# Optimization experiments

Measured on AMD Instinct MI355X. Metric: run time of the kernel, lower is better.

Reference implementation:

```python
import jax, jax.numpy as jnp
import numpy as np

B, D, E, K = 8192, 1024, 8, 5  # batch, in_dim, num_size_classes, num_depth_classes
H = max(64, D)                 # hidden = max(64, in_dim)
EPS = 1e-8


def ordinal_logits_to_probs(logits, num_classes):
    # logits: [B, K-1] cumulative ordinal logits -> [B, K] class probs
    q = jax.nn.sigmoid(logits)
    probs = jnp.concatenate(
        [1.0 - q[:, :1], q[:, :-1] - q[:, 1:], q[:, -1:]], axis=1
    )  # [B, K]
    probs = jnp.clip(probs, EPS)
    return probs / jnp.clip(probs.sum(axis=1, keepdims=True), EPS)


def setup_inputs() -> dict:
    key = jax.random.key(0)
    kx, ks, k1, k2 = jax.random.split(key, 4)
    x = jax.random.normal(kx, (B, D), dtype=jnp.float32)
    size_idx = jax.random.randint(ks, (B,), 0, E, dtype=jnp.int64)
    # per-expert 2-layer MLP params: Linear(D,H) -> ReLU -> Linear(H,K-1)
    W1 = jax.random.normal(k1, (E, D, H), dtype=jnp.float32) / np.sqrt(D)
    b1 = jnp.zeros((E, H), dtype=jnp.float32)
    W2 = jax.random.normal(k2, (E, H, K - 1), dtype=jnp.float32) / np.sqrt(H)
    b2 = jnp.zeros((E, K - 1), dtype=jnp.float32)
    return {"x": x, "size_idx": size_idx, "W1": W1, "b1": b1, "W2": W2, "b2": b2}


def reference(x, size_idx, W1, b1, W2, b2):
    # Hard routing: each token gets the output of expert size_idx[b].
    # Dense all-expert compute + per-token select (same math as mask/gather/scatter,
    # dropout is inference-mode identity).
    h = jax.nn.relu(jnp.einsum('bd,edh->beh', x, W1) + b1)      # [B, E, H]
    all_logits = jnp.einsum('beh,ehk->bek', h, W2) + b2          # [B, E, K-1]
    idx = size_idx.astype(jnp.int32)[:, None, None]              # [B, 1, 1]
    logits = jnp.take_along_axis(all_logits, idx, axis=1)[:, 0]  # [B, K-1]
    probs = ordinal_logits_to_probs(logits, K)                   # [B, K]
    return logits, probs
```

## Files before the change

kernel.cpp:

```cpp
#include <hip/hip_runtime.h>
#include <cstdint>
#include <cstddef>

#define Bn 8192
#define Dn 1024
#define Hn 1024
#define En 8
#define MT 128
#define NB 16
#define MTILES (Bn / MT + En)
#define PERM_N (Bn + En * MT)

typedef unsigned short u16;
typedef __bf16 bf16x8 __attribute__((ext_vector_type(8)));
typedef float f32x4 __attribute__((ext_vector_type(4)));
typedef unsigned short ushort8 __attribute__((ext_vector_type(8)));

__device__ __forceinline__ u16 f2bf(float f) {
  unsigned int u = __float_as_uint(f);
  unsigned int r = u + 0x7fffu + ((u >> 16) & 1u);
  return (u16)(r >> 16);
}

__device__ __forceinline__ void gld16(const void* g, void* l) {
  __builtin_amdgcn_global_load_lds(
      (const __attribute__((address_space(1))) void*)g,
      (__attribute__((address_space(3))) void*)l, 16, 0, 0);
}

#define PIPE_BARRIER_VM4() do {                    \
    asm volatile("" ::: "memory");                 \
    __builtin_amdgcn_s_waitcnt(0x0F74);            \
    __builtin_amdgcn_s_barrier();                  \
    asm volatile("" ::: "memory");                 \
  } while (0)
#define PIPE_BARRIER_VM0() do {                    \
    asm volatile("" ::: "memory");                 \
    __builtin_amdgcn_s_waitcnt(0x0F70);            \
    __builtin_amdgcn_s_barrier();                  \
    asm volatile("" ::: "memory");                 \
  } while (0)

__global__ __launch_bounds__(1024) void route_k(const int* __restrict__ sidx,
                                                int* __restrict__ off,
                                                int* __restrict__ perm) {
  __shared__ int hist[16][En];
  __shared__ int base[16][En];
  __shared__ int eoff[En + 1];
  int t = threadIdx.x;
  int wv = t >> 6;
  if (t < 16 * En) ((int*)hist)[t] = 0;
#pragma unroll
  for (int i = 0; i < PERM_N / 1024; i++) perm[t + i * 1024] = -1;
  __syncthreads();
  int e8[8], r8[8];
#pragma unroll
  for (int i = 0; i < 8; i++) {
    int e = sidx[t + i * 1024];
    e8[i] = e;
    r8[i] = atomicAdd(&hist[wv][e], 1);
  }
  __syncthreads();
  if (t < En) {
    int s = 0;
    for (int w = 0; w < 16; w++) { base[w][t] = s; s += hist[w][t]; }
    hist[0][t] = s;
  }
  __syncthreads();
  if (t == 0) {
    int o = 0;
    for (int e = 0; e < En; e++) {
      eoff[e] = o; off[e] = o;
      o += (hist[0][e] + MT - 1) & ~(MT - 1);
    }
    eoff[En] = o; off[En] = o;
  }
  __syncthreads();
#pragma unroll
  for (int i = 0; i < 8; i++) {
    int e = e8[i];
    perm[eoff[e] + base[wv][e] + r8[i]] = t + i * 1024;
  }
}

__global__ __launch_bounds__(256) void cvt_xp_k(const float* __restrict__ x,
                                                const int* __restrict__ perm,
                                                u16* __restrict__ xbp) {
  size_t idx = ((size_t)blockIdx.x * 256 + threadIdx.x) * 8;
  int p = (int)(idx >> 10);
  int col = (int)(idx & 1023);
  int tok = perm[p];
  ushort8 o;
  if (tok < 0) {
    o = (ushort8){0, 0, 0, 0, 0, 0, 0, 0};
  } else {
    const float* src = x + ((size_t)tok << 10) + col;
    float4 a = *(const float4*)src;
    float4 b = *(const float4*)(src + 4);
    o[0] = f2bf(a.x); o[1] = f2bf(a.y); o[2] = f2bf(a.z); o[3] = f2bf(a.w);
    o[4] = f2bf(b.x); o[5] = f2bf(b.y); o[6] = f2bf(b.z); o[7] = f2bf(b.w);
  }
  *(ushort8*)(xbp + idx) = o;
}

__global__ __launch_bounds__(256) void cvt_w1_k(const float* __restrict__ W1,
                                                u16* __restrict__ W1t) {
  __shared__ float tile[64][65];
  int e = blockIdx.z;
  int k0 = blockIdx.y * 64;
  int n0 = blockIdx.x * 64;
  int c4 = (threadIdx.x & 15) * 4;
  int r0 = threadIdx.x >> 4;
  const float* src = W1 + ((size_t)e << 20) + (size_t)k0 * Hn + n0;
#pragma unroll
  for (int i = 0; i < 4; i++) {
    int r = r0 + i * 16;
    float4 v = *(const float4*)(src + (size_t)r * Hn + c4);
    tile[r][c4 + 0] = v.x; tile[r][c4 + 1] = v.y;
    tile[r][c4 + 2] = v.z; tile[r][c4 + 3] = v.w;
  }
  __syncthreads();
  u16* dst = W1t + ((size_t)e << 20) + (size_t)n0 * Dn + k0;
#pragma unroll
  for (int i = 0; i < 4; i++) {
    int h = r0 + i * 16;
    ushort4 o;
    o.x = f2bf(tile[c4 + 0][h]);
    o.y = f2bf(tile[c4 + 1][h]);
    o.z = f2bf(tile[c4 + 2][h]);
    o.w = f2bf(tile[c4 + 3][h]);
    *(ushort4*)(dst + (size_t)h * Dn + c4) = o;
  }
}

__global__ __launch_bounds__(256) void gemm_k(
    const u16* __restrict__ xbp, const u16* __restrict__ w1t,
    const float* __restrict__ b1, const float* __restrict__ w2,
    const int* __restrict__ off, float* __restrict__ partials) {
  __shared__ u16 As[3][4096];
  __shared__ u16 Bs[3][4096];

  int n0 = blockIdx.x * 128;
  int row0 = blockIdx.y * MT;
  if (row0 >= off[En]) return;
  int e = 0;
  while (row0 >= off[e + 1]) e++;

  int tid = threadIdx.x;
  int lane = tid & 63, w = tid >> 6;
  int wm = w >> 1, wn = w & 1;

  int srow = lane >> 2;
  int slot = lane & 3;
  int scol = (slot ^ ((srow >> 1) & 3)) * 8;
  const u16* aG[2]; const u16* bG[2];
  int lOff[2];
#pragma unroll
  for (int j = 0; j < 2; j++) {
    int rl = 32 * w + 16 * j + srow;
    aG[j] = xbp + (size_t)(row0 + rl) * Dn + scol;
    bG[j] = w1t + ((size_t)e << 20) + (size_t)(n0 + rl) * Dn + scol;
    lOff[j] = (32 * w + 16 * j) * 32;
  }

  f32x4 acc[4][4];
#pragma unroll
  for (int i = 0; i < 4; i++)
#pragma unroll
    for (int j = 0; j < 4; j++)
      acc[i][j] = (f32x4){0.f, 0.f, 0.f, 0.f};

  int fr = lane & 15;
  int qf = lane >> 4;
  int qs = (qf ^ ((fr >> 1) & 3)) * 8;
  int offA[4], offB[4];
#pragma unroll
  for (int i = 0; i < 4; i++)
    offA[i] = (wm * 64 + i * 16 + fr) * 32 + qs;
#pragma unroll
  for (int j = 0; j < 4; j++)
    offB[j] = (wn * 64 + j * 16 + fr) * 32 + qs;

#pragma unroll
  for (int it = 0; it < 2; it++) {
    int ko = it * 32;
    gld16(aG[0] + ko, (u16*)As[it] + lOff[0]);
    gld16(aG[1] + ko, (u16*)As[it] + lOff[1]);
    gld16(bG[0] + ko, (u16*)Bs[it] + lOff[0]);
    gld16(bG[1] + ko, (u16*)Bs[it] + lOff[1]);
  }

#pragma unroll
  for (int i = 0; i < 31; i++) {
    PIPE_BARRIER_VM4();
    if (i + 2 < 32) {
      int s = (i + 2) % 3;
      int ko = (i + 2) * 32;
      gld16(aG[0] + ko, (u16*)As[s] + lOff[0]);
      gld16(aG[1] + ko, (u16*)As[s] + lOff[1]);
      gld16(bG[0] + ko, (u16*)Bs[s] + lOff[0]);
      gld16(bG[1] + ko, (u16*)Bs[s] + lOff[1]);
    }
    const u16* Ab = (const u16*)As[i % 3];
    const u16* Bb = (const u16*)Bs[i % 3];
    bf16x8 af[4], bfr[4];
#pragma unroll
    for (int ii = 0; ii < 4; ii++) af[ii] = *(const bf16x8*)(Ab + offA[ii]);
#pragma unroll
    for (int jj = 0; jj < 4; jj++) bfr[jj] = *(const bf16x8*)(Bb + offB[jj]);
#pragma unroll
    for (int ii = 0; ii < 4; ii++)
#pragma unroll
      for (int jj = 0; jj < 4; jj++)
        acc[ii][jj] = __builtin_amdgcn_mfma_f32_16x16x32_bf16(af[ii], bfr[jj], acc[ii][jj], 0, 0, 0);
  }
  {
    PIPE_BARRIER_VM0();
    const u16* Ab = (const u16*)As[31 % 3];
    const u16* Bb = (const u16*)Bs[31 % 3];
    bf16x8 af[4], bfr[4];
#pragma unroll
    for (int ii = 0; ii < 4; ii++) af[ii] = *(const bf16x8*)(Ab + offA[ii]);
#pragma unroll
    for (int jj = 0; jj < 4; jj++) bfr[jj] = *(const bf16x8*)(Bb + offB[jj]);
#pragma unroll
    for (int ii = 0; ii < 4; ii++)
#pragma unroll
      for (int jj = 0; jj < 4; jj++)
        acc[ii][jj] = __builtin_amdgcn_mfma_f32_16x16x32_bf16(af[ii], bfr[jj], acc[ii][jj], 0, 0, 0);
  }

  int fq = lane >> 4;
  float4 w2v[4]; float b1v[4];
#pragma unroll
  for (int j = 0; j < 4; j++) {
    int col = n0 + wn * 64 + j * 16 + fr;
    w2v[j] = *(const float4*)(w2 + ((size_t)e * Hn + col) * 4);
    b1v[j] = b1[(size_t)e * Hn + col];
  }
  int chunk = blockIdx.x * 2 + wn;
#pragma unroll
  for (int i = 0; i < 4; i++) {
    int rbase = wm * 64 + i * 16 + fq * 4;
#pragma unroll
    for (int r = 0; r < 4; r++) {
      float s0 = 0.f, s1 = 0.f, s2 = 0.f, s3 = 0.f;
#pragma unroll
      for (int j = 0; j < 4; j++) {
        float h = acc[i][j][r] + b1v[j];
        h = fmaxf(h, 0.f);
        s0 = fmaf(h, w2v[j].x, s0);
        s1 = fmaf(h, w2v[j].y, s1);
        s2 = fmaf(h, w2v[j].z, s2);
        s3 = fmaf(h, w2v[j].w, s3);
      }
#pragma unroll
      for (int m = 1; m < 16; m <<= 1) {
        s0 += __shfl_xor(s0, m);
        s1 += __shfl_xor(s1, m);
        s2 += __shfl_xor(s2, m);
        s3 += __shfl_xor(s3, m);
      }
      if (fr == 0) {
        int row = row0 + rbase + r;
        *(float4*)(partials + ((size_t)row * NB + chunk) * 4) =
            make_float4(s0, s1, s2, s3);
      }
    }
  }
}

__global__ void probs_k(const float* __restrict__ partials,
                        const int* __restrict__ perm, const int* __restrict__ off,
                        const int* __restrict__ sidx, const float* __restrict__ b2,
                        float* __restrict__ out) {
  int p = blockIdx.x * blockDim.x + threadIdx.x;
  if (p >= off[En]) return;
  int tok = perm[p];
  if (tok < 0) return;
  int e = sidx[tok];
  float s0 = 0.f, s1 = 0.f, s2 = 0.f, s3 = 0.f;
#pragma unroll
  for (int nb = 0; nb < NB; nb++) {
    float4 v = *(const float4*)(partials + ((size_t)p * NB + nb) * 4);
    s0 += v.x; s1 += v.y; s2 += v.z; s3 += v.w;
  }
  float l0 = s0 + b2[e * 4 + 0];
  float l1 = s1 + b2[e * 4 + 1];
  float l2 = s2 + b2[e * 4 + 2];
  float l3 = s3 + b2[e * 4 + 3];
  out[tok * 4 + 0] = l0; out[tok * 4 + 1] = l1;
  out[tok * 4 + 2] = l2; out[tok * 4 + 3] = l3;
  float q0 = 1.f / (1.f + expf(-l0));
  float q1 = 1.f / (1.f + expf(-l1));
  float q2 = 1.f / (1.f + expf(-l2));
  float q3 = 1.f / (1.f + expf(-l3));
  const float eps = 1e-8f;
  float p0 = fmaxf(1.f - q0, eps);
  float p1 = fmaxf(q0 - q1, eps);
  float p2 = fmaxf(q1 - q2, eps);
  float p3 = fmaxf(q2 - q3, eps);
  float p4 = fmaxf(q3, eps);
  float s = p0 + p1 + p2 + p3 + p4;
  float inv = 1.f / fmaxf(s, eps);
  float* pr = out + (size_t)Bn * 4 + (size_t)tok * 5;
  pr[0] = p0 * inv; pr[1] = p1 * inv; pr[2] = p2 * inv;
  pr[3] = p3 * inv; pr[4] = p4 * inv;
}

extern "C" void kernel_launch(void* const* d_in, const int* in_sizes, int n_in,
                              void* d_out, int out_size, void* d_ws, size_t ws_size,
                              hipStream_t stream) {
  const float* x  = (const float*)d_in[0];
  const int* sidx = (const int*)d_in[1];
  const float* W1 = (const float*)d_in[2];
  const float* b1 = (const float*)d_in[3];
  const float* W2 = (const float*)d_in[4];
  const float* b2 = (const float*)d_in[5];
  float* out = (float*)d_out;

  uint8_t* w = (uint8_t*)d_ws;
  int* off  = (int*)(w + 64);
  int* perm = (int*)(w + 512);
  u16* xbp      = (u16*)(w + 40960);
  u16* w1t      = (u16*)(w + 18919424);
  float* parts  = (float*)(w + 35700736);

  route_k<<<1, 1024, 0, stream>>>(sidx, off, perm);
  cvt_xp_k<<<(PERM_N * Dn) / (256 * 8), 256, 0, stream>>>(x, perm, xbp);
  cvt_w1_k<<<dim3(Hn / 64, Dn / 64, En), 256, 0, stream>>>(W1, w1t);
  gemm_k<<<dim3(Hn / 128, MTILES), 256, 0, stream>>>(xbp, w1t, b1, W2, off, parts);
  probs_k<<<(PERM_N + 255) / 256, 256, 0, stream>>>(parts, perm, off, sidx, b2, out);
}
```

Before: 160.6 us.

## Fuse prep kernels, gather tokens in GEMM, finalize probs via last-block atomics

```diff
diff --git a/kernel.cpp b/kernel.cpp
--- a/kernel.cpp
+++ b/kernel.cpp
@@ -7,9 +7,16 @@
 #define Hn 1024
 #define En 8
 #define MT 128
-#define NB 16
-#define MTILES (Bn / MT + En)
+#define MTILES (PERM_N / MT)
 #define PERM_N (Bn + En * MT)
+
+#define NXB 4096
+#define NWB 2048
+#define NZB 32
+#define XB0 1
+#define WB0 (XB0 + NXB)
+#define ZB0 (WB0 + NWB)
+#define TOTB (ZB0 + NZB)
 
 typedef unsigned short u16;
 typedef __bf16 bf16x8 __attribute__((ext_vector_type(8)));
@@ -41,107 +48,109 @@
     asm volatile("" ::: "memory");                 \
   } while (0)
 
-__global__ __launch_bounds__(1024) void route_k(const int* __restrict__ sidx,
-                                                int* __restrict__ off,
-                                                int* __restrict__ perm) {
-  __shared__ int hist[16][En];
-  __shared__ int base[16][En];
-  __shared__ int eoff[En + 1];
+__global__ __launch_bounds__(256) void prep_k(
+    const float* __restrict__ x, const int* __restrict__ sidx,
+    const float* __restrict__ W1,
+    u16* __restrict__ xb, u16* __restrict__ w1t,
+    int* __restrict__ off, int* __restrict__ perm, int* __restrict__ done,
+    float* __restrict__ out) {
+  int bid = blockIdx.x;
   int t = threadIdx.x;
-  int wv = t >> 6;
-  if (t < 16 * En) ((int*)hist)[t] = 0;
-#pragma unroll
-  for (int i = 0; i < PERM_N / 1024; i++) perm[t + i * 1024] = -1;
-  __syncthreads();
-  int e8[8], r8[8];
-#pragma unroll
-  for (int i = 0; i < 8; i++) {
-    int e = sidx[t + i * 1024];
-    e8[i] = e;
-    r8[i] = atomicAdd(&hist[wv][e], 1);
-  }
-  __syncthreads();
-  if (t < En) {
-    int s = 0;
-    for (int w = 0; w < 16; w++) { base[w][t] = s; s += hist[w][t]; }
-    hist[0][t] = s;
-  }
-  __syncthreads();
-  if (t == 0) {
-    int o = 0;
-    for (int e = 0; e < En; e++) {
-      eoff[e] = o; off[e] = o;
-      o += (hist[0][e] + MT - 1) & ~(MT - 1);
-    }
-    eoff[En] = o; off[En] = o;
-  }
-  __syncthreads();
-#pragma unroll
-  for (int i = 0; i < 8; i++) {
-    int e = e8[i];
-    perm[eoff[e] + base[wv][e] + r8[i]] = t + i * 1024;
-  }
-}
-
-__global__ __launch_bounds__(256) void cvt_xp_k(const float* __restrict__ x,
-                                                const int* __restrict__ perm,
-                                                u16* __restrict__ xbp) {
-  size_t idx = ((size_t)blockIdx.x * 256 + threadIdx.x) * 8;
-  int p = (int)(idx >> 10);
-  int col = (int)(idx & 1023);
-  int tok = perm[p];
-  ushort8 o;
-  if (tok < 0) {
-    o = (ushort8){0, 0, 0, 0, 0, 0, 0, 0};
-  } else {
-    const float* src = x + ((size_t)tok << 10) + col;
+
+  if (bid == 0) {
+    __shared__ int hist[4][En];
+    __shared__ int base[4][En];
+    __shared__ int eoff[En + 1];
+    int wv = t >> 6;
+    if (t < 4 * En) ((int*)hist)[t] = 0;
+    if (t < MTILES) done[t] = 0;
+#pragma unroll
+    for (int i = 0; i < PERM_N / 256; i++) perm[t + i * 256] = -1;
+    __syncthreads();
+    int e32[32], r32[32];
+#pragma unroll
+    for (int i = 0; i < 32; i++) {
+      int e = sidx[t + i * 256];
+      e32[i] = e;
+      r32[i] = atomicAdd(&hist[wv][e], 1);
+    }
+    __syncthreads();
+    if (t < En) {
+      int s = 0;
+      for (int w = 0; w < 4; w++) { base[w][t] = s; s += hist[w][t]; }
+      hist[0][t] = s;
+    }
+    __syncthreads();
+    if (t == 0) {
+      int o = 0;
+      for (int e = 0; e < En; e++) {
+        eoff[e] = o; off[e] = o;
+        o += (hist[0][e] + MT - 1) & ~(MT - 1);
+      }
+      eoff[En] = o; off[En] = o;
+    }
+    __syncthreads();
+#pragma unroll
+    for (int i = 0; i < 32; i++) {
+      int e = e32[i];
+      perm[eoff[e] + base[wv][e] + r32[i]] = t + i * 256;
+    }
+  } else if (bid < WB0) {
+    size_t idx = ((size_t)(bid - XB0) * 256 + t) * 8;
+    const float* src = x + idx;
     float4 a = *(const float4*)src;
     float4 b = *(const float4*)(src + 4);
+    ushort8 o;
     o[0] = f2bf(a.x); o[1] = f2bf(a.y); o[2] = f2bf(a.z); o[3] = f2bf(a.w);
     o[4] = f2bf(b.x); o[5] = f2bf(b.y); o[6] = f2bf(b.z); o[7] = f2bf(b.w);
-  }
-  *(ushort8*)(xbp + idx) = o;
-}
-
-__global__ __launch_bounds__(256) void cvt_w1_k(const float* __restrict__ W1,
-                                                u16* __restrict__ W1t) {
-  __shared__ float tile[64][65];
-  int e = blockIdx.z;
-  int k0 = blockIdx.y * 64;
-  int n0 = blockIdx.x * 64;
-  int c4 = (threadIdx.x & 15) * 4;
-  int r0 = threadIdx.x >> 4;
-  const float* src = W1 + ((size_t)e << 20) + (size_t)k0 * Hn + n0;
-#pragma unroll
-  for (int i = 0; i < 4; i++) {
-    int r = r0 + i * 16;
-    float4 v = *(const float4*)(src + (size_t)r * Hn + c4);
-    tile[r][c4 + 0] = v.x; tile[r][c4 + 1] = v.y;
-    tile[r][c4 + 2] = v.z; tile[r][c4 + 3] = v.w;
-  }
-  __syncthreads();
-  u16* dst = W1t + ((size_t)e << 20) + (size_t)n0 * Dn + k0;
-#pragma unroll
-  for (int i = 0; i < 4; i++) {
-    int h = r0 + i * 16;
-    ushort4 o;
-    o.x = f2bf(tile[c4 + 0][h]);
-    o.y = f2bf(tile[c4 + 1][h]);
-    o.z = f2bf(tile[c4 + 2][h]);
-    o.w = f2bf(tile[c4 + 3][h]);
-    *(ushort4*)(dst + (size_t)h * Dn + c4) = o;
+    *(ushort8*)(xb + idx) = o;
+  } else if (bid < ZB0) {
+    __shared__ float tile[64][65];
+    int wb = bid - WB0;
+    int e = wb >> 8;
+    int k0 = ((wb >> 4) & 15) * 64;
+    int n0 = (wb & 15) * 64;
+    int c4 = (t & 15) * 4;
+    int r0 = t >> 4;
+    const float* src = W1 + ((size_t)e << 20) + (size_t)k0 * Hn + n0;
+#pragma unroll
+    for (int i = 0; i < 4; i++) {
+      int r = r0 + i * 16;
+      float4 v = *(const float4*)(src + (size_t)r * Hn + c4);
+      tile[r][c4 + 0] = v.x; tile[r][c4 + 1] = v.y;
+      tile[r][c4 + 2] = v.z; tile[r][c4 + 3] = v.w;
+    }
+    __syncthreads();
+    u16* dst = w1t + ((size_t)e << 20) + (size_t)n0 * Dn + k0;
+#pragma unroll
+    for (int i = 0; i < 4; i++) {
+      int h = r0 + i * 16;
+      ushort4 o;
+      o.x = f2bf(tile[c4 + 0][h]);
+      o.y = f2bf(tile[c4 + 1][h]);
+      o.z = f2bf(tile[c4 + 2][h]);
+      o.w = f2bf(tile[c4 + 3][h]);
+      *(ushort4*)(dst + (size_t)h * Dn + c4) = o;
+    }
+  } else {
+    size_t idx = ((size_t)(bid - ZB0) * 256 + t) * 4;
+    *(float4*)(out + idx) = make_float4(0.f, 0.f, 0.f, 0.f);
   }
 }
 
 __global__ __launch_bounds__(256) void gemm_k(
-    const u16* __restrict__ xbp, const u16* __restrict__ w1t,
+    const u16* __restrict__ xb, const u16* __restrict__ w1t,
     const float* __restrict__ b1, const float* __restrict__ w2,
-    const int* __restrict__ off, float* __restrict__ partials) {
+    const float* __restrict__ b2,
+    const int* __restrict__ off, const int* __restrict__ perm,
+    int* __restrict__ done, float* __restrict__ out) {
   __shared__ u16 As[3][4096];
   __shared__ u16 Bs[3][4096];
+  __shared__ int sOld;
 
   int n0 = blockIdx.x * 128;
-  int row0 = blockIdx.y * MT;
+  int tb = blockIdx.y;
+  int row0 = tb * MT;
   if (row0 >= off[En]) return;
   int e = 0;
   while (row0 >= off[e + 1]) e++;
@@ -158,7 +167,9 @@
 #pragma unroll
   for (int j = 0; j < 2; j++) {
     int rl = 32 * w + 16 * j + srow;
-    aG[j] = xbp + (size_t)(row0 + rl) * Dn + scol;
+    int tok = perm[row0 + rl];
+    if (tok < 0) tok = 0;
+    aG[j] = xb + ((size_t)tok << 10) + scol;
     bG[j] = w1t + ((size_t)e << 20) + (size_t)(n0 + rl) * Dn + scol;
     lOff[j] = (32 * w + 16 * j) * 32;
   }
@@ -230,7 +241,6 @@
         acc[ii][jj] = __builtin_amdgcn_mfma_f32_16x16x32_bf16(af[ii], bfr[jj], acc[ii][jj], 0, 0, 0);
   }
 
-  int fq = lane >> 4;
   float4 w2v[4]; float b1v[4];
 #pragma unroll
   for (int j = 0; j < 4; j++) {
@@ -238,10 +248,9 @@
     w2v[j] = *(const float4*)(w2 + ((size_t)e * Hn + col) * 4);
     b1v[j] = b1[(size_t)e * Hn + col];
   }
-  int chunk = blockIdx.x * 2 + wn;
 #pragma unroll
   for (int i = 0; i < 4; i++) {
-    int rbase = wm * 64 + i * 16 + fq * 4;
+    int rbase = wm * 64 + i * 16 + qf * 4;
 #pragma unroll
     for (int r = 0; r < 4; r++) {
       float s0 = 0.f, s1 = 0.f, s2 = 0.f, s3 = 0.f;
@@ -262,50 +271,53 @@
         s3 += __shfl_xor(s3, m);
       }
       if (fr == 0) {
-        int row = row0 + rbase + r;
-        *(float4*)(partials + ((size_t)row * NB + chunk) * 4) =
-            make_float4(s0, s1, s2, s3);
-      }
-    }
-  }
-}
-
-__global__ void probs_k(const float* __restrict__ partials,
-                        const int* __restrict__ perm, const int* __restrict__ off,
-                        const int* __restrict__ sidx, const float* __restrict__ b2,
-                        float* __restrict__ out) {
-  int p = blockIdx.x * blockDim.x + threadIdx.x;
-  if (p >= off[En]) return;
-  int tok = perm[p];
-  if (tok < 0) return;
-  int e = sidx[tok];
-  float s0 = 0.f, s1 = 0.f, s2 = 0.f, s3 = 0.f;
-#pragma unroll
-  for (int nb = 0; nb < NB; nb++) {
-    float4 v = *(const float4*)(partials + ((size_t)p * NB + nb) * 4);
-    s0 += v.x; s1 += v.y; s2 += v.z; s3 += v.w;
-  }
-  float l0 = s0 + b2[e * 4 + 0];
-  float l1 = s1 + b2[e * 4 + 1];
-  float l2 = s2 + b2[e * 4 + 2];
-  float l3 = s3 + b2[e * 4 + 3];
-  out[tok * 4 + 0] = l0; out[tok * 4 + 1] = l1;
-  out[tok * 4 + 2] = l2; out[tok * 4 + 3] = l3;
-  float q0 = 1.f / (1.f + expf(-l0));
-  float q1 = 1.f / (1.f + expf(-l1));
-  float q2 = 1.f / (1.f + expf(-l2));
-  float q3 = 1.f / (1.f + expf(-l3));
-  const float eps = 1e-8f;
-  float p0 = fmaxf(1.f - q0, eps);
-  float p1 = fmaxf(q0 - q1, eps);
-  float p2 = fmaxf(q1 - q2, eps);
-  float p3 = fmaxf(q2 - q3, eps);
-  float p4 = fmaxf(q3, eps);
-  float s = p0 + p1 + p2 + p3 + p4;
-  float inv = 1.f / fmaxf(s, eps);
-  float* pr = out + (size_t)Bn * 4 + (size_t)tok * 5;
-  pr[0] = p0 * inv; pr[1] = p1 * inv; pr[2] = p2 * inv;
-  pr[3] = p3 * inv; pr[4] = p4 * inv;
+        int tok = perm[row0 + rbase + r];
+        if (tok >= 0) {
+          float* o = out + (size_t)tok * 4;
+          atomicAdd(o + 0, s0);
+          atomicAdd(o + 1, s1);
+          atomicAdd(o + 2, s2);
+          atomicAdd(o + 3, s3);
+        }
+      }
+    }
+  }
+
+  __syncthreads();
+  if (tid == 0) {
+    __threadfence();
+    sOld = atomicAdd(&done[tb], 1);
+  }
+  __syncthreads();
+  if (sOld == 7) {
+    __threadfence();
+    if (tid < MT) {
+      int tok = perm[row0 + tid];
+      if (tok >= 0) {
+        float l0 = out[tok * 4 + 0] + b2[e * 4 + 0];
+        float l1 = out[tok * 4 + 1] + b2[e * 4 + 1];
+        float l2 = out[tok * 4 + 2] + b2[e * 4 + 2];
+        float l3 = out[tok * 4 + 3] + b2[e * 4 + 3];
+        out[tok * 4 + 0] = l0; out[tok * 4 + 1] = l1;
+        out[tok * 4 + 2] = l2; out[tok * 4 + 3] = l3;
+        float q0 = 1.f / (1.f + expf(-l0));
+        float q1 = 1.f / (1.f + expf(-l1));
+        float q2 = 1.f / (1.f + expf(-l2));
+        float q3 = 1.f / (1.f + expf(-l3));
+        const float eps = 1e-8f;
+        float p0 = fmaxf(1.f - q0, eps);
+        float p1 = fmaxf(q0 - q1, eps);
+        float p2 = fmaxf(q1 - q2, eps);
+        float p3 = fmaxf(q2 - q3, eps);
+        float p4 = fmaxf(q3, eps);
+        float s = p0 + p1 + p2 + p3 + p4;
+        float inv = 1.f / fmaxf(s, eps);
+        float* pr = out + (size_t)Bn * 4 + (size_t)tok * 5;
+        pr[0] = p0 * inv; pr[1] = p1 * inv; pr[2] = p2 * inv;
+        pr[3] = p3 * inv; pr[4] = p4 * inv;
+      }
+    }
+  }
 }
 
 extern "C" void kernel_launch(void* const* d_in, const int* in_sizes, int n_in,
@@ -321,14 +333,12 @@
 
   uint8_t* w = (uint8_t*)d_ws;
   int* off  = (int*)(w + 64);
+  int* done = (int*)(w + 128);
   int* perm = (int*)(w + 512);
-  u16* xbp      = (u16*)(w + 40960);
-  u16* w1t      = (u16*)(w + 18919424);
-  float* parts  = (float*)(w + 35700736);
-
-  route_k<<<1, 1024, 0, stream>>>(sidx, off, perm);
-  cvt_xp_k<<<(PERM_N * Dn) / (256 * 8), 256, 0, stream>>>(x, perm, xbp);
-  cvt_w1_k<<<dim3(Hn / 64, Dn / 64, En), 256, 0, stream>>>(W1, w1t);
-  gemm_k<<<dim3(Hn / 128, MTILES), 256, 0, stream>>>(xbp, w1t, b1, W2, off, parts);
-  probs_k<<<(PERM_N + 255) / 256, 256, 0, stream>>>(parts, perm, off, sidx, b2, out);
-}
+  u16* xb   = (u16*)(w + 40960);
+  u16* w1t  = (u16*)(w + 40960 + 16777216);
+
+  prep_k<<<TOTB, 256, 0, stream>>>(x, sidx, W1, xb, w1t, off, perm, done, out);
+  gemm_k<<<dim3(Hn / 128, MTILES), 256, 0, stream>>>(xb, w1t, b1, W2, b2,
+                                                     off, perm, done, out);
+}
```

After: 226.0 us. 1.41x slower.
